# Performance work log

Measured on AMD Instinct MI355X. Metric: run time of the kernel, lower is better.

Reference implementation:

```python
import jax, jax.numpy as jnp
import numpy as np
import itertools

LN_EPS = 1e-5

def _combo_idx(d):
    # lexicographic (i<j) and (i<j<k) combination indices, matching the torch nested loops
    pairs = np.array(list(itertools.combinations(range(d), 2)), dtype=np.int32)  # [P,2]
    trips = np.array(list(itertools.combinations(range(d), 3)), dtype=np.int32)  # [T,3]
    return pairs, trips

def setup_inputs() -> dict:
    key = jax.random.key(0)
    k1, k2 = jax.random.split(key)
    d, batch, out_dim = 64, 4096, 512
    total = d + d * (d - 1) // 2 + d * (d - 1) * (d - 2) // 6  # 63744
    x = jax.random.normal(k1, (batch, d), dtype=jnp.float32)
    W = jax.random.normal(k2, (total, out_dim), dtype=jnp.float32) * (1.0 / np.sqrt(total))
    b = jnp.zeros((out_dim,), dtype=jnp.float32)
    gamma = jnp.ones((out_dim,), dtype=jnp.float32)
    beta = jnp.zeros((out_dim,), dtype=jnp.float32)
    return {"x": x, "W": W, "b": b, "gamma": gamma, "beta": beta}

def reference(x, W, b, gamma, beta):
    d = x.shape[1]
    pairs, trips = _combo_idx(d)  # static numpy index tables
    # pairwise products x_i * x_j for i<j  -> [B, C(d,2)]
    pw = x[:, pairs[:, 0]] * x[:, pairs[:, 1]]
    # triplet products x_i * x_j * x_k for i<j<k -> [B, C(d,3)]
    tp = x[:, trips[:, 0]] * x[:, trips[:, 1]] * x[:, trips[:, 2]]
    feats = jnp.concatenate([x, pw, tp], axis=1)  # [B, total]
    h = feats @ W + b  # Linear
    # LayerNorm over last dim
    mu = jnp.mean(h, axis=-1, keepdims=True)
    var = jnp.var(h, axis=-1, keepdims=True)
    hn = (h - mu) * jax.lax.rsqrt(var + LN_EPS) * gamma + beta
    return jax.nn.relu(hn)
```

## Files before the change

kernel.cpp:

```cpp
#include <hip/hip_runtime.h>
#include <stdint.h>

#define D 64
#define KTOT 43744
#define NPAIR 2016
#define NOUT 512
#define MROWS 4096
#define BM 128
#define BN 256
#define BK 32
#define NSTEPS (KTOT / BK)
#define K2B (KTOT * 2)

typedef __attribute__((ext_vector_type(8))) short short8;
typedef __attribute__((ext_vector_type(4))) float f32x4;
typedef __attribute__((ext_vector_type(4))) uint32_t u32x4;

__device__ __forceinline__ uint32_t cvtpk(float lo, float hi) {
  uint32_t r;
  asm("v_cvt_pk_bf16_f32 %0, %1, %2" : "=v"(r) : "v"(lo), "v"(hi));
  return r;
}

__device__ __forceinline__ void unrank(int k, int& i, int& j, int& l) {
  if (k < D) {
    i = k; j = D; l = D;
  } else if (k < D + NPAIR) {
    int p = k - D;
    i = 0;
    while (p >= D - 1 - i) { p -= D - 1 - i; ++i; }
    j = i + 1 + p; l = D;
  } else {
    int t = k - (D + NPAIR);
    i = 0;
    for (;;) { int c = (D - 1 - i) * (D - 2 - i) / 2; if (t < c) break; t -= c; ++i; }
    j = i + 1;
    while (t >= D - 1 - j) { t -= D - 1 - j; ++j; }
    l = j + 1 + t;
  }
}

__device__ __forceinline__ bool inc_idx(int& i, int& j, int& l) {
  if (l >= D) {
    if (j >= D) { ++i; if (i == D) { i = 0; j = 1; } return true; }
    ++j;
    if (j == D) { ++i; j = i + 1; if (j == D) { i = 0; j = 1; l = 2; } }
    return true;
  }
  ++l;
  if (l == D) {
    ++j; l = j + 1;
    if (l == D) { ++i; j = i + 1; l = j + 1; }
    return true;
  }
  return false;
}

__global__ void build_idx_k(uint32_t* __restrict__ idx) {
  int k = blockIdx.x * 256 + threadIdx.x;
  if (k >= KTOT) return;
  int i, j, l;
  unrank(k, i, j, l);
  idx[k] = (uint32_t)i | ((uint32_t)j << 8) | ((uint32_t)l << 16);
}

__global__ void wtrans_k(const float* __restrict__ W, char* __restrict__ Wt) {
  __shared__ float tile[64][65];
  int bk = blockIdx.x;
  int bn = blockIdx.y;
  int t = threadIdx.x;
  int k0 = bk * 64, n0 = bn * 64;
  int col = t & 63, r0 = t >> 6;
  #pragma unroll
  for (int p = 0; p < 16; ++p) {
    int row = p * 4 + r0;
    tile[col][row] = (k0 + row < KTOT) ? W[(size_t)(k0 + row) * NOUT + (n0 + col)] : 0.0f;
  }
  __syncthreads();
  for (int u = t; u < 512; u += 256) {
    int n = u >> 3, s8 = u & 7;
    int kc0 = k0 + s8 * 8;
    if (kc0 >= KTOT) continue;
    int ng = n0 + n;
    int b = s8 * 8;
    u32x4 v = {cvtpk(tile[n][b + 0], tile[n][b + 1]),
               cvtpk(tile[n][b + 2], tile[n][b + 3]),
               cvtpk(tile[n][b + 4], tile[n][b + 5]),
               cvtpk(tile[n][b + 6], tile[n][b + 7])};
    *(u32x4*)(Wt + (size_t)ng * K2B + (size_t)kc0 * 2) = v;
  }
}

template<int USE_WT, int USE_IDX>
__global__ void __launch_bounds__(512, 4)
gemm_k(const float* __restrict__ x, const float* __restrict__ W,
       const char* __restrict__ Wt, const uint32_t* __restrict__ idxg,
       float* __restrict__ part, int S, int Slog, int steps_per, int swz) {
  __shared__ float XmT[D * 128];
  __shared__ __align__(16) char Al[2][BM * 64];

  const int t = threadIdx.x;
  const int lane = t & 63;
  const int w = t >> 6;

  int mb, ns;
  if (swz) {
    int xcd = blockIdx.x & 7;
    int sub = blockIdx.x >> 3;
    ns = xcd + 8 * (sub >> 5);
    mb = sub & 31;
  } else {
    mb = blockIdx.x & 31;
    ns = blockIdx.x >> 5;
  }
  const int nb = ns >> Slog;
  const int sb = ns & (S - 1);

  {
    int m = t >> 2, i0 = (t & 3) * 16;
    const float* src = x + (size_t)(mb * BM + m) * D + i0;
    #pragma unroll
    for (int c = 0; c < 4; ++c) {
      f32x4 v = *(const f32x4*)(src + c * 4);
      #pragma unroll
      for (int e = 0; e < 4; ++e) XmT[(i0 + c * 4 + e) * 128 + m] = v[e];
    }
  }

  f32x4 acc[4][4];
  #pragma unroll
  for (int a = 0; a < 4; ++a)
    #pragma unroll
    for (int b = 0; b < 4; ++b) {
      f32x4 z = {0.f, 0.f, 0.f, 0.f};
      acc[a][b] = z;
    }

  const int wr = w >> 2, wc = w & 3;
  const int g = lane >> 4;

  int Abase[4];
  #pragma unroll
  for (int fm = 0; fm < 4; ++fm) {
    int m = wr * 64 + fm * 16 + (lane & 15);
    Abase[fm] = m * 64 + ((g ^ ((m >> 1) & 3)) << 4);
  }

  const int fg_m = t & 127;
  const int fg_kh = t >> 7;
  const float* xcol = XmT + fg_m;
  const uint32_t Awr = (uint32_t)(fg_m * 64 + ((fg_kh ^ ((fg_m >> 1) & 3)) << 4));

  const int ks0 = sb * steps_per;
  const int ks1 = (ks0 + steps_per < NSTEPS) ? (ks0 + steps_per) : NSTEPS;

  auto gen_a = [&](int ks, int buf) {
    uint32_t pk[4];
    const int kbase = ks * BK + fg_kh * 8;
    if (USE_IDX) {
      if (kbase >= D + NPAIR) {
        const u32x4* ip = (const u32x4*)(idxg + kbase);
        u32x4 I0 = ip[0], I1 = ip[1];
        uint32_t prev = 0xFFFFFFFFu;
        float pp = 0.0f;
        float fv[8];
        #pragma unroll
        for (int e = 0; e < 8; ++e) {
          uint32_t uu = __builtin_amdgcn_readfirstlane(e < 4 ? I0[e & 3] : I1[e & 3]);
          uint32_t ij = uu & 0xFFFFu;
          if (ij != prev) {
            pp = xcol[(uu & 63u) * 128] * xcol[((uu >> 8) & 63u) * 128];
            prev = ij;
          }
          fv[e] = pp * xcol[((uu >> 16) & 63u) * 128];
        }
        #pragma unroll
        for (int c = 0; c < 4; ++c) pk[c] = cvtpk(fv[2 * c], fv[2 * c + 1]);
      } else {
        const u32x4* ip = (const u32x4*)(idxg + kbase);
        u32x4 I0 = ip[0], I1 = ip[1];
        float fv[8];
        #pragma unroll
        for (int e = 0; e < 8; ++e) {
          uint32_t uu = (e < 4) ? I0[e & 3] : I1[e & 3];
          uint32_t ji = (uu >> 8) & 0xFFu, li = uu >> 16;
          float xi = xcol[(uu & 63u) * 128];
          float xj = (ji < 64u) ? xcol[(ji & 63u) * 128] : 1.0f;
          float xl = (li < 64u) ? xcol[(li & 63u) * 128] : 1.0f;
          fv[e] = xi * xj * xl;
        }
        #pragma unroll
        for (int c = 0; c < 4; ++c) pk[c] = cvtpk(fv[2 * c], fv[2 * c + 1]);
      }
    } else {
      int ii, jj, ll;
      unrank(kbase, ii, jj, ll);
      float fv[8];
      #pragma unroll
      for (int h = 0; h < 8; ++h) {
        float xi = xcol[(ii & 63) * 128];
        float xj = (jj < 64) ? xcol[(jj & 63) * 128] : 1.0f;
        float xl = (ll < 64) ? xcol[(ll & 63) * 128] : 1.0f;
        fv[h] = xi * xj * xl;
        if (h < 7) inc_idx(ii, jj, ll);
      }
      #pragma unroll
      for (int c = 0; c < 4; ++c) pk[c] = cvtpk(fv[2 * c], fv[2 * c + 1]);
    }
    u32x4 v0 = {pk[0], pk[1], pk[2], pk[3]};
    *(u32x4*)(&Al[buf][0] + Awr) = v0;
  };

  if constexpr (USE_WT) {
    const char* Bp[4];
    #pragma unroll
    for (int fn = 0; fn < 4; ++fn) {
      int row = nb * BN + wc * 64 + fn * 16 + (lane & 15);
      Bp[fn] = Wt + (size_t)row * K2B + ((uint32_t)g << 4);
    }

    gen_a(ks0, 0);
    __syncthreads();

    int cur = 0;
    for (int ks = ks0; ks < ks1; ++ks) {
      const bool more = (ks + 1 < ks1);
      short8 bv[4];
      {
        const size_t ko = (size_t)(ks * BK) * 2;
        #pragma unroll
        for (int fn = 0; fn < 4; ++fn)
          bv[fn] = *(const short8*)(Bp[fn] + ko);
      }
      if (more) gen_a(ks + 1, cur ^ 1);

      __builtin_amdgcn_s_setprio(1);
      short8 av[4];
      #pragma unroll
      for (int fm = 0; fm < 4; ++fm)
        av[fm] = *(const short8*)(&Al[cur][0] + Abase[fm]);
      #pragma unroll
      for (int fm = 0; fm < 4; ++fm)
        #pragma unroll
        for (int fn = 0; fn < 4; ++fn)
          acc[fm][fn] = __builtin_amdgcn_mfma_f32_16x16x32_bf16(av[fm], bv[fn], acc[fm][fn], 0, 0, 0);
      __builtin_amdgcn_s_setprio(0);

      if (more) __syncthreads();
      cur ^= 1;
    }
  } else {
    __shared__ __align__(16) char Bl[2][BN * 64];
    int Bbase[4];
    #pragma unroll
    for (int fn = 0; fn < 4; ++fn) {
      int n = wc * 64 + fn * 16 + (lane & 15);
      Bbase[fn] = n * 64 + ((g ^ ((n >> 1) & 3)) << 4);
    }
    auto stage_b = [&](int ks, int buf) {
      const int k0 = ks * BK;
      #pragma unroll
      for (int i2 = 0; i2 < 2; ++i2) {
        int u = t + i2 * 512;
        int n = u & 255, s = u >> 8;
        const float* wp = W + (size_t)(k0 + s * 8) * NOUT + nb * BN + n;
        float f[8];
        #pragma unroll
        for (int e = 0; e < 8; ++e) f[e] = wp[(size_t)e * NOUT];
        u32x4 v = {cvtpk(f[0], f[1]), cvtpk(f[2], f[3]),
                   cvtpk(f[4], f[5]), cvtpk(f[6], f[7])};
        *(u32x4*)(&Bl[buf][0] + n * 64 + ((s ^ ((n >> 1) & 3)) << 4)) = v;
      }
    };

    stage_b(ks0, 0);
    gen_a(ks0, 0);
    __syncthreads();

    int cur = 0;
    for (int ks = ks0; ks < ks1; ++ks) {
      const bool more = (ks + 1 < ks1);
      if (more) { stage_b(ks + 1, cur ^ 1); gen_a(ks + 1, cur ^ 1); }

      __builtin_amdgcn_s_setprio(1);
      short8 av[4], bv[4];
      #pragma unroll
      for (int fm = 0; fm < 4; ++fm)
        av[fm] = *(const short8*)(&Al[cur][0] + Abase[fm]);
      #pragma unroll
      for (int fn = 0; fn < 4; ++fn)
        bv[fn] = *(const short8*)(&Bl[cur][0] + Bbase[fn]);
      #pragma unroll
      for (int fm = 0; fm < 4; ++fm)
        #pragma unroll
        for (int fn = 0; fn < 4; ++fn)
          acc[fm][fn] = __builtin_amdgcn_mfma_f32_16x16x32_bf16(av[fm], bv[fn], acc[fm][fn], 0, 0, 0);
      __builtin_amdgcn_s_setprio(0);

      if (more) __syncthreads();
      cur ^= 1;
    }
  }

  #pragma unroll
  for (int fm = 0; fm < 4; ++fm) {
    int rbase = mb * BM + wr * 64 + fm * 16 + ((lane >> 4) << 2);
    #pragma unroll
    for (int fn = 0; fn < 4; ++fn) {
      int col = nb * BN + wc * 64 + fn * 16 + (lane & 15);
      float* dst = part + ((size_t)sb * MROWS + rbase) * NOUT + col;
      #pragma unroll
      for (int r = 0; r < 4; ++r) dst[(size_t)r * NOUT] = acc[fm][fn][r];
    }
  }
}

__global__ void ln_k(const float* part, int S,
                     const float* __restrict__ bias, const float* __restrict__ gamma,
                     const float* __restrict__ beta, float* out) {
  int row = blockIdx.x;
  int t = threadIdx.x;
  float v[2];
  #pragma unroll
  for (int q = 0; q < 2; ++q) {
    int c = t + q * 256;
    float s = bias[c];
    for (int sbi = 0; sbi < S; ++sbi)
      s += part[((size_t)sbi * MROWS + row) * NOUT + c];
    v[q] = s;
  }
  float sum = v[0] + v[1];
  float sq = v[0] * v[0] + v[1] * v[1];
  #pragma unroll
  for (int off = 32; off > 0; off >>= 1) {
    sum += __shfl_xor(sum, off, 64);
    sq  += __shfl_xor(sq, off, 64);
  }
  __shared__ float red[8];
  int wv = t >> 6;
  if ((t & 63) == 0) { red[wv] = sum; red[4 + wv] = sq; }
  __syncthreads();
  sum = red[0] + red[1] + red[2] + red[3];
  sq  = red[4] + red[5] + red[6] + red[7];
  float mu = sum * (1.0f / NOUT);
  float var = sq * (1.0f / NOUT) - mu * mu;
  float rs = rsqrtf(var + 1e-5f);
  #pragma unroll
  for (int q = 0; q < 2; ++q) {
    int c = t + q * 256;
    float hn = (v[q] - mu) * rs * gamma[c] + beta[c];
    out[(size_t)row * NOUT + c] = fmaxf(hn, 0.0f);
  }
}

extern "C" void kernel_launch(void* const* d_in, const int* in_sizes, int n_in,
                              void* d_out, int out_size, void* d_ws, size_t ws_size,
                              hipStream_t stream) {
  const float* x     = (const float*)d_in[0];
  const float* W     = (const float*)d_in[1];
  const float* bias  = (const float*)d_in[2];
  const float* gamma = (const float*)d_in[3];
  const float* beta  = (const float*)d_in[4];
  float* out = (float*)d_out;
  (void)in_sizes; (void)n_in; (void)out_size;

  const size_t IDXB = 262144;
  const size_t WTB  = (size_t)NOUT * K2B;
  const size_t PART = (size_t)MROWS * NOUT * sizeof(float);

  char* base = (char*)d_ws;
  uint32_t* idx = (uint32_t*)base;
  char* Wt = base + IDXB;

  const bool has_idx = ws_size >= IDXB;
  bool use_wt = false;
  int S = 1, Slog = 0;
  if (ws_size >= IDXB + WTB + 8 * PART)      { use_wt = true;  S = 8; Slog = 3; }
  else if (ws_size >= IDXB + 8 * PART)       { use_wt = false; S = 8; Slog = 3; }
  else if (ws_size >= IDXB + WTB + 4 * PART) { use_wt = true;  S = 4; Slog = 2; }
  else if (ws_size >= IDXB + 4 * PART)       { use_wt = false; S = 4; Slog = 2; }
  else if (ws_size >= IDXB + WTB + 2 * PART) { use_wt = true;  S = 2; Slog = 1; }
  else if (ws_size >= IDXB + 2 * PART)       { use_wt = false; S = 2; Slog = 1; }
  else if (ws_size >= IDXB + WTB)            { use_wt = true;  S = 1; Slog = 0; }

  float* part = out;
  if (S > 1) part = (float*)(base + IDXB + (use_wt ? WTB : 0));

  int steps_per = (NSTEPS + S - 1) / S;
  int grid = 32 * (NOUT / BN) * S;
  int swz = (grid == 512) ? 1 : 0;

  if (has_idx) build_idx_k<<<(KTOT + 255) / 256, 256, 0, stream>>>(idx);
  if (use_wt)  wtrans_k<<<dim3((KTOT + 63) / 64, 8), 256, 0, stream>>>(W, Wt);

  if (use_wt)
    gemm_k<1, 1><<<grid, 512, 0, stream>>>(x, W, Wt, idx, part, S, Slog, steps_per, swz);
  else if (has_idx)
    gemm_k<0, 1><<<grid, 512, 0, stream>>>(x, W, Wt, idx, part, S, Slog, steps_per, swz);
  else
    gemm_k<0, 0><<<grid, 512, 0, stream>>>(x, W, Wt, nullptr, part, S, Slog, steps_per, swz);

  ln_k<<<MROWS, 256, 0, stream>>>(part, S, bias, gamma, beta, out);
}
```

Measured before the change: 317.9 us.

## Double K-tile to 64 with padded K and unified triplet feature generation

Raises the K step from 32 to 64, padding K to a multiple of 64 with sentinel index entries that point at a constant-one row in shared memory and with zero-filled weights. Each thread now builds 16 features per step through one unified pair-reuse path, replacing the separate linear/pair/triplet branches. LDS tiles are widened with an 8-way XOR swizzle, and each step issues two MFMA rounds per barrier. The aim is to halve barrier and loop overhead per unit of work, at the cost of more LDS and registers, which may lower occupancy.

```diff
diff --git a/kernel.cpp b/kernel.cpp
--- a/kernel.cpp
+++ b/kernel.cpp
@@ -8,9 +8,10 @@
 #define MROWS 4096
 #define BM 128
 #define BN 256
-#define BK 32
-#define NSTEPS (KTOT / BK)
-#define K2B (KTOT * 2)
+#define BK 64
+#define NSTEPS ((KTOT + BK - 1) / BK)
+#define KPAD (NSTEPS * BK)
+#define K2B (KPAD * 2)
 
 typedef __attribute__((ext_vector_type(8))) short short8;
 typedef __attribute__((ext_vector_type(4))) float f32x4;
@@ -40,25 +41,10 @@
   }
 }
 
-__device__ __forceinline__ bool inc_idx(int& i, int& j, int& l) {
-  if (l >= D) {
-    if (j >= D) { ++i; if (i == D) { i = 0; j = 1; } return true; }
-    ++j;
-    if (j == D) { ++i; j = i + 1; if (j == D) { i = 0; j = 1; l = 2; } }
-    return true;
-  }
-  ++l;
-  if (l == D) {
-    ++j; l = j + 1;
-    if (l == D) { ++i; j = i + 1; l = j + 1; }
-    return true;
-  }
-  return false;
-}
-
 __global__ void build_idx_k(uint32_t* __restrict__ idx) {
   int k = blockIdx.x * 256 + threadIdx.x;
-  if (k >= KTOT) return;
+  if (k >= KPAD) return;
+  if (k >= KTOT) { idx[k] = 64u | (64u << 8) | (64u << 16); return; }
   int i, j, l;
   unrank(k, i, j, l);
   idx[k] = (uint32_t)i | ((uint32_t)j << 8) | ((uint32_t)l << 16);
@@ -79,15 +65,13 @@
   __syncthreads();
   for (int u = t; u < 512; u += 256) {
     int n = u >> 3, s8 = u & 7;
-    int kc0 = k0 + s8 * 8;
-    if (kc0 >= KTOT) continue;
     int ng = n0 + n;
     int b = s8 * 8;
     u32x4 v = {cvtpk(tile[n][b + 0], tile[n][b + 1]),
                cvtpk(tile[n][b + 2], tile[n][b + 3]),
                cvtpk(tile[n][b + 4], tile[n][b + 5]),
                cvtpk(tile[n][b + 6], tile[n][b + 7])};
-    *(u32x4*)(Wt + (size_t)ng * K2B + (size_t)kc0 * 2) = v;
+    *(u32x4*)(Wt + (size_t)ng * K2B + (size_t)(k0 + b) * 2) = v;
   }
 }
 
@@ -96,8 +80,8 @@
 gemm_k(const float* __restrict__ x, const float* __restrict__ W,
        const char* __restrict__ Wt, const uint32_t* __restrict__ idxg,
        float* __restrict__ part, int S, int Slog, int steps_per, int swz) {
-  __shared__ float XmT[D * 128];
-  __shared__ __align__(16) char Al[2][BM * 64];
+  __shared__ float XmT[65 * 128];
+  __shared__ __align__(16) char Al[2][BM * 128];
 
   const int t = threadIdx.x;
   const int lane = t & 63;
@@ -125,7 +109,9 @@
       #pragma unroll
       for (int e = 0; e < 4; ++e) XmT[(i0 + c * 4 + e) * 128 + m] = v[e];
     }
-  }
+    if (t < 128) XmT[64 * 128 + t] = 1.0f;
+  }
+  __syncthreads();
 
   f32x4 acc[4][4];
   #pragma unroll
@@ -143,72 +129,62 @@
   #pragma unroll
   for (int fm = 0; fm < 4; ++fm) {
     int m = wr * 64 + fm * 16 + (lane & 15);
-    Abase[fm] = m * 64 + ((g ^ ((m >> 1) & 3)) << 4);
+    Abase[fm] = m * 128 + ((g ^ (m & 7)) << 4);
   }
 
   const int fg_m = t & 127;
   const int fg_kh = t >> 7;
   const float* xcol = XmT + fg_m;
-  const uint32_t Awr = (uint32_t)(fg_m * 64 + ((fg_kh ^ ((fg_m >> 1) & 3)) << 4));
+  const uint32_t Awr0 = (uint32_t)(fg_m * 128 + (((fg_kh * 2 + 0) ^ (fg_m & 7)) << 4));
+  const uint32_t Awr1 = (uint32_t)(fg_m * 128 + (((fg_kh * 2 + 1) ^ (fg_m & 7)) << 4));
 
   const int ks0 = sb * steps_per;
   const int ks1 = (ks0 + steps_per < NSTEPS) ? (ks0 + steps_per) : NSTEPS;
 
   auto gen_a = [&](int ks, int buf) {
-    uint32_t pk[4];
-    const int kbase = ks * BK + fg_kh * 8;
+    const int kbase = ks * BK + fg_kh * 16;
+    u32x4 I0, I1, I2, I3;
     if (USE_IDX) {
-      if (kbase >= D + NPAIR) {
-        const u32x4* ip = (const u32x4*)(idxg + kbase);
-        u32x4 I0 = ip[0], I1 = ip[1];
-        uint32_t prev = 0xFFFFFFFFu;
-        float pp = 0.0f;
-        float fv[8];
-        #pragma unroll
-        for (int e = 0; e < 8; ++e) {
-          uint32_t uu = __builtin_amdgcn_readfirstlane(e < 4 ? I0[e & 3] : I1[e & 3]);
-          uint32_t ij = uu & 0xFFFFu;
-          if (ij != prev) {
-            pp = xcol[(uu & 63u) * 128] * xcol[((uu >> 8) & 63u) * 128];
-            prev = ij;
-          }
-          fv[e] = pp * xcol[((uu >> 16) & 63u) * 128];
-        }
-        #pragma unroll
-        for (int c = 0; c < 4; ++c) pk[c] = cvtpk(fv[2 * c], fv[2 * c + 1]);
-      } else {
-        const u32x4* ip = (const u32x4*)(idxg + kbase);
-        u32x4 I0 = ip[0], I1 = ip[1];
-        float fv[8];
-        #pragma unroll
-        for (int e = 0; e < 8; ++e) {
-          uint32_t uu = (e < 4) ? I0[e & 3] : I1[e & 3];
-          uint32_t ji = (uu >> 8) & 0xFFu, li = uu >> 16;
-          float xi = xcol[(uu & 63u) * 128];
-          float xj = (ji < 64u) ? xcol[(ji & 63u) * 128] : 1.0f;
-          float xl = (li < 64u) ? xcol[(li & 63u) * 128] : 1.0f;
-          fv[e] = xi * xj * xl;
-        }
-        #pragma unroll
-        for (int c = 0; c < 4; ++c) pk[c] = cvtpk(fv[2 * c], fv[2 * c + 1]);
-      }
+      const u32x4* ip = (const u32x4*)(idxg + kbase);
+      I0 = ip[0]; I1 = ip[1]; I2 = ip[2]; I3 = ip[3];
     } else {
-      int ii, jj, ll;
-      unrank(kbase, ii, jj, ll);
-      float fv[8];
-      #pragma unroll
-      for (int h = 0; h < 8; ++h) {
-        float xi = xcol[(ii & 63) * 128];
-        float xj = (jj < 64) ? xcol[(jj & 63) * 128] : 1.0f;
-        float xl = (ll < 64) ? xcol[(ll & 63) * 128] : 1.0f;
-        fv[h] = xi * xj * xl;
-        if (h < 7) inc_idx(ii, jj, ll);
-      }
-      #pragma unroll
-      for (int c = 0; c < 4; ++c) pk[c] = cvtpk(fv[2 * c], fv[2 * c + 1]);
-    }
-    u32x4 v0 = {pk[0], pk[1], pk[2], pk[3]};
-    *(u32x4*)(&Al[buf][0] + Awr) = v0;
+      #pragma unroll
+      for (int q = 0; q < 16; ++q) {
+        int k = kbase + q;
+        int i, j, l;
+        if (k < KTOT) unrank(k, i, j, l); else { i = 64; j = 64; l = 64; }
+        uint32_t uu = (uint32_t)i | ((uint32_t)j << 8) | ((uint32_t)l << 16);
+        if (q < 4) I0[q] = uu; else if (q < 8) I1[q - 4] = uu;
+        else if (q < 12) I2[q - 8] = uu; else I3[q - 12] = uu;
+      }
+    }
+    float fv[16];
+    {
+      uint32_t prev = 0xFFFFFFFFu; float pp = 0.0f;
+      #pragma unroll
+      for (int e = 0; e < 8; ++e) {
+        uint32_t uu = (e < 4) ? I0[e & 3] : I1[e & 3];
+        uint32_t ij = uu & 0xFFFFu;
+        if (ij != prev) { pp = xcol[(uu & 127u) * 128] * xcol[((uu >> 8) & 127u) * 128]; prev = ij; }
+        fv[e] = pp * xcol[((uu >> 16) & 127u) * 128];
+      }
+    }
+    {
+      uint32_t prev = 0xFFFFFFFFu; float pp = 0.0f;
+      #pragma unroll
+      for (int e = 0; e < 8; ++e) {
+        uint32_t uu = (e < 4) ? I2[e & 3] : I3[e & 3];
+        uint32_t ij = uu & 0xFFFFu;
+        if (ij != prev) { pp = xcol[(uu & 127u) * 128] * xcol[((uu >> 8) & 127u) * 128]; prev = ij; }
+        fv[8 + e] = pp * xcol[((uu >> 16) & 127u) * 128];
+      }
+    }
+    u32x4 v0 = {cvtpk(fv[0], fv[1]), cvtpk(fv[2], fv[3]),
+                cvtpk(fv[4], fv[5]), cvtpk(fv[6], fv[7])};
+    u32x4 v1 = {cvtpk(fv[8], fv[9]), cvtpk(fv[10], fv[11]),
+                cvtpk(fv[12], fv[13]), cvtpk(fv[14], fv[15])};
+    *(u32x4*)(&Al[buf][0] + Awr0) = v0;
+    *(u32x4*)(&Al[buf][0] + Awr1) = v1;
   };
 
   if constexpr (USE_WT) {
@@ -225,13 +201,11 @@
     int cur = 0;
     for (int ks = ks0; ks < ks1; ++ks) {
       const bool more = (ks + 1 < ks1);
-      short8 bv[4];
-      {
-        const size_t ko = (size_t)(ks * BK) * 2;
-        #pragma unroll
-        for (int fn = 0; fn < 4; ++fn)
-          bv[fn] = *(const short8*)(Bp[fn] + ko);
-      }
+      const size_t ko = (size_t)(ks * BK) * 2;
+      short8 bv0[4];
+      #pragma unroll
+      for (int fn = 0; fn < 4; ++fn) bv0[fn] = *(const short8*)(Bp[fn] + ko);
+
       if (more) gen_a(ks + 1, cur ^ 1);
 
       __builtin_amdgcn_s_setprio(1);
@@ -239,37 +213,49 @@
       #pragma unroll
       for (int fm = 0; fm < 4; ++fm)
         av[fm] = *(const short8*)(&Al[cur][0] + Abase[fm]);
+      short8 bv1[4];
+      #pragma unroll
+      for (int fn = 0; fn < 4; ++fn) bv1[fn] = *(const short8*)(Bp[fn] + ko + 64);
       #pragma unroll
       for (int fm = 0; fm < 4; ++fm)
         #pragma unroll
         for (int fn = 0; fn < 4; ++fn)
-          acc[fm][fn] = __builtin_amdgcn_mfma_f32_16x16x32_bf16(av[fm], bv[fn], acc[fm][fn], 0, 0, 0);
+          acc[fm][fn] = __builtin_amdgcn_mfma_f32_16x16x32_bf16(av[fm], bv0[fn], acc[fm][fn], 0, 0, 0);
+      #pragma unroll
+      for (int fm = 0; fm < 4; ++fm)
+        av[fm] = *(const short8*)(&Al[cur][0] + (Abase[fm] ^ 0x40));
+      #pragma unroll
+      for (int fm = 0; fm < 4; ++fm)
+        #pragma unroll
+        for (int fn = 0; fn < 4; ++fn)
+          acc[fm][fn] = __builtin_amdgcn_mfma_f32_16x16x32_bf16(av[fm], bv1[fn], acc[fm][fn], 0, 0, 0);
       __builtin_amdgcn_s_setprio(0);
 
       if (more) __syncthreads();
       cur ^= 1;
     }
   } else {
-    __shared__ __align__(16) char Bl[2][BN * 64];
+    __shared__ __align__(16) char Bl[2][BN * 128];
     int Bbase[4];
     #pragma unroll
     for (int fn = 0; fn < 4; ++fn) {
       int n = wc * 64 + fn * 16 + (lane & 15);
-      Bbase[fn] = n * 64 + ((g ^ ((n >> 1) & 3)) << 4);
+      Bbase[fn] = n * 128 + ((g ^ (n & 7)) << 4);
     }
     auto stage_b = [&](int ks, int buf) {
       const int k0 = ks * BK;
       #pragma unroll
-      for (int i2 = 0; i2 < 2; ++i2) {
+      for (int i2 = 0; i2 < 4; ++i2) {
         int u = t + i2 * 512;
         int n = u & 255, s = u >> 8;
         const float* wp = W + (size_t)(k0 + s * 8) * NOUT + nb * BN + n;
         float f[8];
         #pragma unroll
-        for (int e = 0; e < 8; ++e) f[e] = wp[(size_t)e * NOUT];
+        for (int e = 0; e < 8; ++e)
+          f[e] = (k0 + s * 8 + e < KTOT) ? wp[(size_t)e * NOUT] : 0.0f;
         u32x4 v = {cvtpk(f[0], f[1]), cvtpk(f[2], f[3]),
                    cvtpk(f[4], f[5]), cvtpk(f[6], f[7])};
-        *(u32x4*)(&Bl[buf][0] + n * 64 + ((s ^ ((n >> 1) & 3)) << 4)) = v;
+        *(u32x4*)(&Bl[buf][0] + n * 128 + ((s ^ (n & 7)) << 4)) = v;
       }
     };
 
@@ -283,18 +269,21 @@
       if (more) { stage_b(ks + 1, cur ^ 1); gen_a(ks + 1, cur ^ 1); }
 
       __builtin_amdgcn_s_setprio(1);
-      short8 av[4], bv[4];
-      #pragma unroll
-      for (int fm = 0; fm < 4; ++fm)
-        av[fm] = *(const short8*)(&Al[cur][0] + Abase[fm]);
-      #pragma unroll
-      for (int fn = 0; fn < 4; ++fn)
-        bv[fn] = *(const short8*)(&Bl[cur][0] + Bbase[fn]);
-      #pragma unroll
-      for (int fm = 0; fm < 4; ++fm)
+      #pragma unroll
+      for (int kc = 0; kc < 2; ++kc) {
+        short8 av[4], bv[4];
+        #pragma unroll
+        for (int fm = 0; fm < 4; ++fm)
+          av[fm] = *(const short8*)(&Al[cur][0] + (Abase[fm] ^ (kc << 6)));
         #pragma unroll
         for (int fn = 0; fn < 4; ++fn)
-          acc[fm][fn] = __builtin_amdgcn_mfma_f32_16x16x32_bf16(av[fm], bv[fn], acc[fm][fn], 0, 0, 0);
+          bv[fn] = *(const short8*)(&Bl[cur][0] + (Bbase[fn] ^ (kc << 6)));
+        #pragma unroll
+        for (int fm = 0; fm < 4; ++fm)
+          #pragma unroll
+          for (int fn = 0; fn < 4; ++fn)
+            acc[fm][fn] = __builtin_amdgcn_mfma_f32_16x16x32_bf16(av[fm], bv[fn], acc[fm][fn], 0, 0, 0);
+      }
       __builtin_amdgcn_s_setprio(0);
 
       if (more) __syncthreads();
@@ -390,8 +379,8 @@
   int grid = 32 * (NOUT / BN) * S;
   int swz = (grid == 512) ? 1 : 0;
 
-  if (has_idx) build_idx_k<<<(KTOT + 255) / 256, 256, 0, stream>>>(idx);
-  if (use_wt)  wtrans_k<<<dim3((KTOT + 63) / 64, 8), 256, 0, stream>>>(W, Wt);
+  if (has_idx) build_idx_k<<<(KPAD + 255) / 256, 256, 0, stream>>>(idx);
+  if (use_wt)  wtrans_k<<<dim3(NSTEPS, 8), 256, 0, stream>>>(W, Wt);
 
   if (use_wt)
     gemm_k<1, 1><<<grid, 512, 0, stream>>>(x, W, Wt, idx, part, S, Slog, steps_per, swz);
```

After: 485.0 us. 1.53x slower.
